# Kernel optimization log

Measured on AMD Instinct MI355X. Metric: run time of the kernel, lower is better.

The kernel has to match this reference:

```python
import jax, jax.numpy as jnp
import numpy as np

B, H, W, C = 8, 64, 64, 256
C8 = C // 8  # query/key channels


def setup_inputs() -> dict:
    key = jax.random.key(0)
    ks = jax.random.split(key, 8)
    s = 0.02  # init scale for weights
    return {
        "x": jax.random.normal(ks[0], (B, H, W, C), dtype=jnp.float32),
        "Wq": jax.random.normal(ks[1], (C, C8), dtype=jnp.float32) * s,
        "bq": jnp.zeros((C8,), dtype=jnp.float32),
        "Wk": jax.random.normal(ks[2], (C, C8), dtype=jnp.float32) * s,
        "bk": jnp.zeros((C8,), dtype=jnp.float32),
        "Wv": jax.random.normal(ks[3], (C, C), dtype=jnp.float32) * s,
        "bv": jnp.zeros((C,), dtype=jnp.float32),
        "gamma": jnp.full((1,), 0.5, dtype=jnp.float32),
    }


def reference(x, Wq, bq, Wk, bk, Wv, bv, gamma):
    Bn, Hn, Wn, Cn = x.shape
    N = Hn * Wn
    xf = x.reshape(Bn, N, Cn)            # flatten spatial dims: [B, N, C]
    # 1x1 convs == per-pixel dense projections over channels
    q = xf @ Wq + bq                     # [B, N, C//8]
    k = xf @ Wk + bk                     # [B, N, C//8]
    v = xf @ Wv + bv                     # [B, N, C]
    # energy[b,i,j] = k_i . q_j  (matches tf.matmul(key, query, transpose_b=True))
    energy = jnp.einsum('bic,bjc->bij', k, q)   # [B, N, N]
    attn = jax.nn.softmax(energy, axis=-1)      # softmax over last axis
    # out_i = sum_j attn[i,j] * v_j  (intended SAGAN aggregation in NHWC layout)
    out = jnp.einsum('bij,bjc->bic', attn, v)   # [B, N, C]
    out = out.reshape(Bn, Hn, Wn, Cn)
    return gamma * out + x
```

## Files before the change

### kernel.cpp

```cpp
#include <hip/hip_runtime.h>

typedef __attribute__((ext_vector_type(8))) short short8;
typedef __attribute__((ext_vector_type(4))) float f32x4;
typedef __attribute__((ext_vector_type(16))) float f32x16;
typedef __attribute__((ext_vector_type(2))) unsigned int u32x2;
typedef __attribute__((ext_vector_type(4))) unsigned int u32x4;
typedef unsigned short u16;
typedef unsigned int u32;

#define MFMA16(a, b, c) __builtin_amdgcn_mfma_f32_16x16x32_bf16((a), (b), (c), 0, 0, 0)
#define MFMA32(a, b, c) __builtin_amdgcn_mfma_f32_32x32x16_bf16((a), (b), (c), 0, 0, 0)

#define BAR_VMEM() asm volatile("s_waitcnt vmcnt(0) lgkmcnt(0)\ns_barrier" ::: "memory")
#define BAR_LDS()  asm volatile("s_waitcnt lgkmcnt(0)\ns_barrier" ::: "memory")

#define BATCH 8
#define NTOK 4096
#define CDIM 256
#define CQK 32
#define LOG2E 1.4426950408889634f

__device__ __forceinline__ u16 f2bf(float f) {
  u32 u = __float_as_uint(f);
  return (u16)((u + 0x7FFFu + ((u >> 16) & 1u)) >> 16);
}
__device__ __forceinline__ u32 pack2(float a, float b) {
  const u32 ua = __float_as_uint(a) + 0x8000u;
  const u32 ub = __float_as_uint(b) + 0x8000u;
#if __has_builtin(__builtin_amdgcn_perm)
  return __builtin_amdgcn_perm(ub, ua, 0x07060302u);
#else
  return (ua >> 16) | (ub & 0xFFFF0000u);
#endif
}
__device__ __forceinline__ float fexp2(float x) {
#if __has_builtin(__builtin_amdgcn_exp2f)
  return __builtin_amdgcn_exp2f(x);
#else
  return exp2f(x);
#endif
}
__device__ __forceinline__ void gl_lds16(const u16* g, u16* l) {
  __builtin_amdgcn_global_load_lds(
      (const __attribute__((address_space(1))) unsigned int*)(g),
      (__attribute__((address_space(3))) unsigned int*)(l), 16, 0, 0);
}

__global__ void k_prep(const float* __restrict__ Wq, const float* __restrict__ bq,
                       const float* __restrict__ Wk, const float* __restrict__ bk,
                       const float* __restrict__ Wv, const float* __restrict__ bv,
                       u16* __restrict__ wtf, float* __restrict__ bias) {
  const int f = blockIdx.x;
  const int L = threadIdx.x;
  const int ct = f >> 3, ks = f & 7;
  const int o = ct * 16 + (L & 15);
  const int ch = ks * 32 + (L >> 4) * 8;
  short8 v8;
#pragma unroll
  for (int jj = 0; jj < 8; jj++) {
    const int c = ch + jj;
    float v;
    if (o < 32)       v = Wq[c * CQK + o];
    else if (o < 64)  v = Wk[c * CQK + (o - 32)];
    else              v = Wv[c * CDIM + (o - 64)];
    v8[jj] = (short)f2bf(v);
  }
  *(short8*)(wtf + (size_t)f * 512 + L * 8) = v8;
  if (f == 0) {
    for (int i = L; i < 320; i += 64) {
      if (i < 32)      bias[i] = bq[i];
      else if (i < 64) bias[i] = bk[i - 32];
      else             bias[i] = bv[i - 64];
    }
  }
}

__global__ __launch_bounds__(256, 2) void k_proj(
    const float* __restrict__ x, const u16* __restrict__ wtf,
    const float* __restrict__ bias,
    u16* __restrict__ q_ws, u16* __restrict__ k_ws, u16* __restrict__ vt_ws) {
  __shared__ u16 x_lds[64 * 264];
  __shared__ u16 vt_t[64 * 72];
  const int m0 = blockIdx.x * 64;
  const int tid = threadIdx.x;
  const int w = tid >> 6, L = tid & 63;
  const int lr = L & 15, q4 = L >> 4;

  short8 wfA[5], wfB[5];
#pragma unroll
  for (int j = 0; j < 5; j++)
    wfA[j] = *(const short8*)(wtf + ((size_t)((j * 4 + w) * 8 + 0)) * 512 + L * 8);

#pragma unroll
  for (int ii = 0; ii < 8; ii++) {
    const int e = (tid + 256 * ii) * 8;
    const int row = e >> 8, col = e & 255;
    const float* src = x + (size_t)(m0 + row) * CDIM + col;
    f32x4 a = *(const f32x4*)src;
    f32x4 b4 = *(const f32x4*)(src + 4);
    u32x4 pk;
    pk[0] = pack2(a[0], a[1]);
    pk[1] = pack2(a[2], a[3]);
    pk[2] = pack2(b4[0], b4[1]);
    pk[3] = pack2(b4[2], b4[3]);
    *(u32x4*)&x_lds[row * 264 + col] = pk;
  }
  __syncthreads();

  f32x4 acc[4][5];
#pragma unroll
  for (int rg = 0; rg < 4; rg++)
#pragma unroll
    for (int j = 0; j < 5; j++) acc[rg][j] = (f32x4){0.f, 0.f, 0.f, 0.f};

#pragma unroll
  for (int ks = 0; ks < 8; ks++) {
    if (ks < 7) {
#pragma unroll
      for (int j = 0; j < 5; j++) {
        short8 v = *(const short8*)(wtf +
            ((size_t)((j * 4 + w) * 8 + ks + 1)) * 512 + L * 8);
        if (ks & 1) wfA[j] = v; else wfB[j] = v;
      }
    }
#pragma unroll
    for (int rg = 0; rg < 4; rg++) {
      short8 a = *(const short8*)&x_lds[(rg * 16 + lr) * 264 + ks * 32 + q4 * 8];
#pragma unroll
      for (int j = 0; j < 5; j++)
        acc[rg][j] = MFMA16(a, (ks & 1) ? wfB[j] : wfA[j], acc[rg][j]);
    }
  }

  {
    const float bb = bias[w * 16 + lr];
#pragma unroll
    for (int rg = 0; rg < 4; rg++)
#pragma unroll
      for (int r = 0; r < 4; r++) {
        const int row = m0 + rg * 16 + q4 * 4 + r;
        float v = acc[rg][0][r] + bb;
        if (w < 2) q_ws[(size_t)row * CQK + w * 16 + lr] = f2bf(v);
        else       k_ws[(size_t)row * CQK + (w - 2) * 16 + lr] = f2bf(v * LOG2E);
      }
  }
  const int b = m0 >> 12, nloc = m0 & 4095;
  const int rb2 = ((lr >> 3) & 1) << 2;
  const int c_l = w * 16 + lr;
#pragma unroll
  for (int cg = 0; cg < 4; cg++) {
    __syncthreads();
    const int j = cg + 1;
    const float bb = bias[(4 + cg * 4 + w) * 16 + lr];
#pragma unroll
    for (int rg = 0; rg < 4; rg++) {
      const int n_base = (rg * 16 + q4 * 4) ^ rb2;
      u32x2 pk;
      pk[0] = pack2(acc[rg][j][0] + bb, acc[rg][j][1] + bb);
      pk[1] = pack2(acc[rg][j][2] + bb, acc[rg][j][3] + bb);
      *(u32x2*)&vt_t[c_l * 72 + n_base] = pk;
    }
    __syncthreads();
#pragma unroll
    for (int i = 0; i < 2; i++) {
      const int gch = tid + 256 * i;
      const int cl2 = gch >> 3, jc = gch & 7;
      short8 v = *(const short8*)&vt_t[cl2 * 72 + jc * 8];
      *(short8*)(vt_ws + ((size_t)(b * CDIM + cg * 64 + cl2)) * NTOK + nloc + jc * 8) = v;
    }
  }
}

__global__ __launch_bounds__(256, 2) void k_attn(
    const float* __restrict__ x, const u16* __restrict__ q_ws,
    const u16* __restrict__ k_ws, const u16* __restrict__ vt_ws,
    const float* __restrict__ gamma, float* __restrict__ out) {
  __shared__ u16 vt_lds[2][256 * 64];
  __shared__ u16 p_lds[64 * 64];

  const int bid = blockIdx.x;
  const int b = bid & 7;
  const int it = bid >> 3;
  const int i0 = it * 64;
  const int tid = threadIdx.x;
  const int w = tid >> 6, L = tid & 63;
  const int lr = L & 15, q4 = L >> 4;
  const int L31 = L & 31, Lhi = L >> 5, L7 = L & 7;

  const short8 a_k = *(const short8*)(k_ws +
      ((size_t)(b * NTOK + i0 + w * 16 + lr)) * CQK + q4 * 8);

  const int cl_base = tid >> 3;
  const int jc_sw = (tid & 7) ^ (cl_base & 7);
  const u16* vt_g = vt_ws + ((size_t)(b * CDIM + cl_base)) * NTOK + jc_sw * 8;
  const u16* q_base = q_ws + (size_t)b * NTOK * CQK;

  f32x16 o_acc[2][2];
#pragma unroll
  for (int ih = 0; ih < 2; ih++)
#pragma unroll
    for (int ct2 = 0; ct2 < 2; ct2++)
#pragma unroll
      for (int e = 0; e < 16; e++) o_acc[ih][ct2][e] = 0.f;
  float lsum = 0.f;

  u16* pw0 = p_lds + (w * 16 + lr) * 64 + (((q4 & 1) ^ ((lr >> 3) & 1)) << 2);
  const int q4h = q4 >> 1;

  short8 bqA[4], bqB[4];
#pragma unroll
  for (int t = 0; t < 4; t++)
    bqA[t] = *(const short8*)(q_base + (size_t)(t * 16 + lr) * CQK + q4 * 8);
#pragma unroll
  for (int ii = 0; ii < 8; ii++)
    gl_lds16(vt_g + (size_t)(ii * 32) * NTOK, &vt_lds[0][ii * 2048 + w * 512]);

#define ATTN_ITER(JT, VB_CUR, VB_NXT, BQ, BQN)                                   \
  do {                                                                           \
    const int j0 = (JT) * 64;                                                    \
    BAR_LDS();                         \
                             \
    f32x4 s[4];                                                                  \
    _Pragma("unroll")                                                            \
    for (int t = 0; t < 4; t++)                                                  \
      s[t] = MFMA16(BQ[t], a_k, ((f32x4){0.f, 0.f, 0.f, 0.f}));                  \
                   \
    _Pragma("unroll")                                                            \
    for (int t = 0; t < 4; t++) {                                                \
      const float p0 = fexp2(s[t][0]);                                           \
      const float p1 = fexp2(s[t][1]);                                           \
      const float p2 = fexp2(s[t][2]);                                           \
      const float p3 = fexp2(s[t][3]);                                           \
      lsum += (p0 + p1) + (p2 + p3);                                             \
      u32x2 pk;                                                                  \
      pk[0] = pack2(p0, p1);                                                     \
      pk[1] = pack2(p2, p3);                                                     \
      *(u32x2*)(pw0 + (((2 * t + q4h) ^ (lr & 7)) * 8)) = pk;                    \
    }                                                                            \
    BAR_VMEM();          \
             \
    if ((JT) < 63) {                                                             \
      _Pragma("unroll")                                                          \
      for (int ii = 0; ii < 8; ii++)                                             \
        gl_lds16(vt_g + (size_t)(ii * 32) * NTOK + (j0 + 64),                    \
                 &VB_NXT[ii * 2048 + w * 512]);                                  \
    }                                                                            \
    _Pragma("unroll")                                                            \
    for (int t = 0; t < 4; t++)                                                  \
      BQN[t] = *(const short8*)(q_base +                                         \
               (size_t)(j0 + 64 + t * 16 + lr) * CQK + q4 * 8);                  \
             \
    _Pragma("unroll")                                                            \
    for (int ks = 0; ks < 4; ks++) {                                             \
      const int slot = (((ks * 2 + Lhi) ^ L7)) * 8;                              \
      short8 a_p0 = *(const short8*)(p_lds + L31 * 64 + slot);                   \
      short8 a_p1 = *(const short8*)(p_lds + (32 + L31) * 64 + slot);            \
      _Pragma("unroll")                                                          \
      for (int ct2 = 0; ct2 < 2; ct2++) {                                        \
        const int cl = w * 64 + ct2 * 32 + L31;                                  \
        short8 b_v = *(const short8*)(VB_CUR + cl * 64 + slot);                  \
        o_acc[0][ct2] = MFMA32(a_p0, b_v, o_acc[0][ct2]);                        \
        o_acc[1][ct2] = MFMA32(a_p1, b_v, o_acc[1][ct2]);                        \
      }                                                                          \
    }                                                                            \
  } while (0)

  for (int jt2 = 0; jt2 < 64; jt2 += 2) {
    ATTN_ITER(jt2,     vt_lds[0], vt_lds[1], bqA, bqB);
    ATTN_ITER(jt2 + 1, vt_lds[1], vt_lds[0], bqB, bqA);
  }
#undef ATTN_ITER

  float s2 = lsum;
  s2 += __shfl_xor(s2, 16);
  s2 += __shfl_xor(s2, 32);
  const float rl = 1.0f / s2;
  BAR_LDS();
  float* lp = (float*)p_lds;
  if (q4 == 0) lp[w * 16 + lr] = rl;
  BAR_LDS();

  float linv2[2][16];
#pragma unroll
  for (int ih = 0; ih < 2; ih++)
#pragma unroll
    for (int rg = 0; rg < 16; rg++)
      linv2[ih][rg] = lp[ih * 32 + (rg & 3) + 8 * (rg >> 2) + 4 * Lhi];

  const float g = gamma[0];
#pragma unroll
  for (int ih = 0; ih < 2; ih++)
#pragma unroll
    for (int ct2 = 0; ct2 < 2; ct2++) {
      const int c = w * 64 + ct2 * 32 + L31;
#pragma unroll
      for (int rg = 0; rg < 16; rg++) {
        const int i = i0 + ih * 32 + (rg & 3) + 8 * (rg >> 2) + 4 * Lhi;
        const size_t idx = ((size_t)(b * NTOK + i)) * CDIM + c;
        out[idx] = g * (o_acc[ih][ct2][rg] * linv2[ih][rg]) + x[idx];
      }
    }
}

extern "C" void kernel_launch(void* const* d_in, const int* in_sizes, int n_in,
                              void* d_out, int out_size, void* d_ws, size_t ws_size,
                              hipStream_t stream) {
  const float* x  = (const float*)d_in[0];
  const float* Wq = (const float*)d_in[1];
  const float* bq = (const float*)d_in[2];
  const float* Wk = (const float*)d_in[3];
  const float* bk = (const float*)d_in[4];
  const float* Wv = (const float*)d_in[5];
  const float* bv = (const float*)d_in[6];
  const float* gamma = (const float*)d_in[7];
  float* out = (float*)d_out;

  char* ws = (char*)d_ws;
  u16* q_ws  = (u16*)(ws);
  u16* k_ws  = (u16*)(ws + (2u << 20));
  u16* vt_ws = (u16*)(ws + (4u << 20));
  u16* wtf   = (u16*)(ws + (20u << 20));
  float* bias = (float*)(ws + (20u << 20) + (256u << 10));

  k_prep<<<160, 64, 0, stream>>>(Wq, bq, Wk, bk, Wv, bv, wtf, bias);
  k_proj<<<512, 256, 0, stream>>>(x, wtf, bias, q_ws, k_ws, vt_ws);
  k_attn<<<512, 256, 0, stream>>>(x, q_ws, k_ws, vt_ws, gamma, out);
}
```

Baseline: 196.8 us.

## Software-pipeline QK^T/exp of next tile with PV MFMAs via double-buffered P

Double-buffers the P tile in LDS so the score MFMAs and exp/pack for tile j+1 are interleaved with the PV MFMA loop of tile j. This drops one barrier per iteration and lets VALU exp work overlap matrix-core work. Adds a prologue and epilogue and an extra 8KB of LDS, which could affect occupancy at 2 blocks per CU.

```diff
diff --git a/kernel.cpp b/kernel.cpp
--- a/kernel.cpp
+++ b/kernel.cpp
@@ -176,7 +176,7 @@
     const u16* __restrict__ k_ws, const u16* __restrict__ vt_ws,
     const float* __restrict__ gamma, float* __restrict__ out) {
   __shared__ u16 vt_lds[2][256 * 64];
-  __shared__ u16 p_lds[64 * 64];
+  __shared__ u16 p_lds[2][64 * 64];
 
   const int bid = blockIdx.x;
   const int b = bid & 7;
@@ -204,8 +204,23 @@
       for (int e = 0; e < 16; e++) o_acc[ih][ct2][e] = 0.f;
   float lsum = 0.f;
 
-  u16* pw0 = p_lds + (w * 16 + lr) * 64 + (((q4 & 1) ^ ((lr >> 3) & 1)) << 2);
+  const int pw_off = (w * 16 + lr) * 64 + (((q4 & 1) ^ ((lr >> 3) & 1)) << 2);
   const int q4h = q4 >> 1;
+  u16* const pl0 = &p_lds[0][0];
+  u16* const pl1 = &p_lds[1][0];
+
+#define EXPW(SV, T, PW)                                                          \
+  do {                                                                           \
+    const float p0 = fexp2((SV)[0]);                                             \
+    const float p1 = fexp2((SV)[1]);                                             \
+    const float p2 = fexp2((SV)[2]);                                             \
+    const float p3 = fexp2((SV)[3]);                                             \
+    lsum += (p0 + p1) + (p2 + p3);                                               \
+    u32x2 pk;                                                                    \
+    pk[0] = pack2(p0, p1);                                                       \
+    pk[1] = pack2(p2, p3);                                                       \
+    *(u32x2*)((PW) + (((2 * (T) + q4h) ^ (lr & 7)) * 8)) = pk;                   \
+  } while (0)
 
   short8 bqA[4], bqB[4];
 #pragma unroll
@@ -214,69 +229,90 @@
 #pragma unroll
   for (int ii = 0; ii < 8; ii++)
     gl_lds16(vt_g + (size_t)(ii * 32) * NTOK, &vt_lds[0][ii * 2048 + w * 512]);
-
-#define ATTN_ITER(JT, VB_CUR, VB_NXT, BQ, BQN)                                   \
+  {
+    f32x4 s0 = MFMA16(bqA[0], a_k, ((f32x4){0.f, 0.f, 0.f, 0.f}));
+    f32x4 s1 = MFMA16(bqA[1], a_k, ((f32x4){0.f, 0.f, 0.f, 0.f}));
+    f32x4 s2 = MFMA16(bqA[2], a_k, ((f32x4){0.f, 0.f, 0.f, 0.f}));
+    f32x4 s3 = MFMA16(bqA[3], a_k, ((f32x4){0.f, 0.f, 0.f, 0.f}));
+    u16* pwn = pl0 + pw_off;
+    EXPW(s0, 0, pwn);
+    EXPW(s1, 1, pwn);
+    EXPW(s2, 2, pwn);
+    EXPW(s3, 3, pwn);
+  }
+#pragma unroll
+  for (int t = 0; t < 4; t++)
+    bqB[t] = *(const short8*)(q_base + (size_t)(64 + t * 16 + lr) * CQK + q4 * 8);
+
+#define ATTN_ITER(JT, PL_CUR, PL_NXT, VB_CUR, VB_NXT, BQN, BQF, DO_Q)            \
   do {                                                                           \
     const int j0 = (JT) * 64;                                                    \
-    BAR_LDS();                         \
-                             \
-    f32x4 s[4];                                                                  \
+    BAR_VMEM();    \
     _Pragma("unroll")                                                            \
-    for (int t = 0; t < 4; t++)                                                  \
-      s[t] = MFMA16(BQ[t], a_k, ((f32x4){0.f, 0.f, 0.f, 0.f}));                  \
-                   \
-    _Pragma("unroll")                                                            \
-    for (int t = 0; t < 4; t++) {                                                \
-      const float p0 = fexp2(s[t][0]);                                           \
-      const float p1 = fexp2(s[t][1]);                                           \
-      const float p2 = fexp2(s[t][2]);                                           \
-      const float p3 = fexp2(s[t][3]);                                           \
-      lsum += (p0 + p1) + (p2 + p3);                                             \
-      u32x2 pk;                                                                  \
-      pk[0] = pack2(p0, p1);                                                     \
-      pk[1] = pack2(p2, p3);                                                     \
-      *(u32x2*)(pw0 + (((2 * t + q4h) ^ (lr & 7)) * 8)) = pk;                    \
-    }                                                                            \
-    BAR_VMEM();          \
-             \
-    if ((JT) < 63) {                                                             \
-      _Pragma("unroll")                                                          \
-      for (int ii = 0; ii < 8; ii++)                                             \
-        gl_lds16(vt_g + (size_t)(ii * 32) * NTOK + (j0 + 64),                    \
-                 &VB_NXT[ii * 2048 + w * 512]);                                  \
-    }                                                                            \
-    _Pragma("unroll")                                                            \
-    for (int t = 0; t < 4; t++)                                                  \
-      BQN[t] = *(const short8*)(q_base +                                         \
-               (size_t)(j0 + 64 + t * 16 + lr) * CQK + q4 * 8);                  \
-             \
+    for (int ii = 0; ii < 8; ii++)                                               \
+      gl_lds16(vt_g + (size_t)(ii * 32) * NTOK + (j0 + 64),                      \
+               &VB_NXT[ii * 2048 + w * 512]);                                    \
+       \
+    f32x4 s0 = MFMA16(BQN[0], a_k, ((f32x4){0.f, 0.f, 0.f, 0.f}));               \
+    f32x4 s1 = MFMA16(BQN[1], a_k, ((f32x4){0.f, 0.f, 0.f, 0.f}));               \
+    f32x4 s2 = MFMA16(BQN[2], a_k, ((f32x4){0.f, 0.f, 0.f, 0.f}));               \
+    f32x4 s3 = MFMA16(BQN[3], a_k, ((f32x4){0.f, 0.f, 0.f, 0.f}));               \
+    u16* pwn = (PL_NXT) + pw_off;                                                \
+            \
     _Pragma("unroll")                                                            \
     for (int ks = 0; ks < 4; ks++) {                                             \
       const int slot = (((ks * 2 + Lhi) ^ L7)) * 8;                              \
-      short8 a_p0 = *(const short8*)(p_lds + L31 * 64 + slot);                   \
-      short8 a_p1 = *(const short8*)(p_lds + (32 + L31) * 64 + slot);            \
+      short8 a_p0 = *(const short8*)((PL_CUR) + L31 * 64 + slot);                \
+      short8 a_p1 = *(const short8*)((PL_CUR) + (32 + L31) * 64 + slot);         \
       _Pragma("unroll")                                                          \
       for (int ct2 = 0; ct2 < 2; ct2++) {                                        \
         const int cl = w * 64 + ct2 * 32 + L31;                                  \
-        short8 b_v = *(const short8*)(VB_CUR + cl * 64 + slot);                  \
+        short8 b_v = *(const short8*)((VB_CUR) + cl * 64 + slot);                \
         o_acc[0][ct2] = MFMA32(a_p0, b_v, o_acc[0][ct2]);                        \
         o_acc[1][ct2] = MFMA32(a_p1, b_v, o_acc[1][ct2]);                        \
       }                                                                          \
+      if (ks == 0) EXPW(s0, 0, pwn);                                             \
+      if (ks == 1) EXPW(s1, 1, pwn);                                             \
+      if (ks == 2) EXPW(s2, 2, pwn);                                             \
+      if (ks == 3) EXPW(s3, 3, pwn);                                             \
+    }                                                                            \
+    if (DO_Q) {                                                                  \
+      _Pragma("unroll")                                                          \
+      for (int t = 0; t < 4; t++)                                                \
+        BQF[t] = *(const short8*)(q_base +                                       \
+                 (size_t)(j0 + 128 + t * 16 + lr) * CQK + q4 * 8);               \
     }                                                                            \
   } while (0)
 
-  for (int jt2 = 0; jt2 < 64; jt2 += 2) {
-    ATTN_ITER(jt2,     vt_lds[0], vt_lds[1], bqA, bqB);
-    ATTN_ITER(jt2 + 1, vt_lds[1], vt_lds[0], bqB, bqA);
-  }
+  for (int jt2 = 0; jt2 < 62; jt2 += 2) {
+    ATTN_ITER(jt2,     pl0, pl1, (&vt_lds[0][0]), (&vt_lds[1][0]), bqB, bqA, 1);
+    ATTN_ITER(jt2 + 1, pl1, pl0, (&vt_lds[1][0]), (&vt_lds[0][0]), bqA, bqB, 1);
+  }
+  ATTN_ITER(62, pl0, pl1, (&vt_lds[0][0]), (&vt_lds[1][0]), bqB, bqA, 0);
 #undef ATTN_ITER
+
+  BAR_VMEM();
+#pragma unroll
+  for (int ks = 0; ks < 4; ks++) {
+    const int slot = (((ks * 2 + Lhi) ^ L7)) * 8;
+    short8 a_p0 = *(const short8*)(pl1 + L31 * 64 + slot);
+    short8 a_p1 = *(const short8*)(pl1 + (32 + L31) * 64 + slot);
+#pragma unroll
+    for (int ct2 = 0; ct2 < 2; ct2++) {
+      const int cl = w * 64 + ct2 * 32 + L31;
+      short8 b_v = *(const short8*)(&vt_lds[1][0] + cl * 64 + slot);
+      o_acc[0][ct2] = MFMA32(a_p0, b_v, o_acc[0][ct2]);
+      o_acc[1][ct2] = MFMA32(a_p1, b_v, o_acc[1][ct2]);
+    }
+  }
+#undef EXPW
 
   float s2 = lsum;
   s2 += __shfl_xor(s2, 16);
   s2 += __shfl_xor(s2, 32);
   const float rl = 1.0f / s2;
   BAR_LDS();
-  float* lp = (float*)p_lds;
+  float* lp = (float*)pl0;
   if (q4 == 0) lp[w * 16 + lr] = rl;
   BAR_LDS();
 
```

Result: no change. 195.3 us (-0.8%).

## Drop LDS staging in attention; prepack V into MFMA fragment layout

Applied to the files above, without the earlier changes.

The projection kernel now writes V in a pre-swizzled per-fragment layout, so the attention kernel can load MFMA B operands straight from global memory into registers. The attention loop computes scores with 32x32 MFMAs, exponentiates them and feeds P directly as the A operand from registers. This removes the P and V round trips through LDS and all per-iteration barriers. Each wave computes its own scores redundantly instead of sharing them, and the change depends on global load latency being hidden by register prefetching.

```diff
diff --git a/kernel.cpp b/kernel.cpp
--- a/kernel.cpp
+++ b/kernel.cpp
@@ -10,9 +10,6 @@
 
 #define MFMA16(a, b, c) __builtin_amdgcn_mfma_f32_16x16x32_bf16((a), (b), (c), 0, 0, 0)
 #define MFMA32(a, b, c) __builtin_amdgcn_mfma_f32_32x32x16_bf16((a), (b), (c), 0, 0, 0)
-
-#define BAR_VMEM() asm volatile("s_waitcnt vmcnt(0) lgkmcnt(0)\ns_barrier" ::: "memory")
-#define BAR_LDS()  asm volatile("s_waitcnt lgkmcnt(0)\ns_barrier" ::: "memory")
 
 #define BATCH 8
 #define NTOK 4096
@@ -39,11 +36,6 @@
 #else
   return exp2f(x);
 #endif
-}
-__device__ __forceinline__ void gl_lds16(const u16* g, u16* l) {
-  __builtin_amdgcn_global_load_lds(
-      (const __attribute__((address_space(1))) unsigned int*)(g),
-      (__attribute__((address_space(3))) unsigned int*)(l), 16, 0, 0);
 }
 
 __global__ void k_prep(const float* __restrict__ Wq, const float* __restrict__ bq,
@@ -80,7 +72,7 @@
     const float* __restrict__ bias,
     u16* __restrict__ q_ws, u16* __restrict__ k_ws, u16* __restrict__ vt_ws) {
   __shared__ u16 x_lds[64 * 264];
-  __shared__ u16 vt_t[64 * 72];
+  __shared__ u16 vt_t[64 * 76];
   const int m0 = blockIdx.x * 64;
   const int tid = threadIdx.x;
   const int w = tid >> 6, L = tid & 63;
@@ -144,8 +136,7 @@
         else       k_ws[(size_t)row * CQK + (w - 2) * 16 + lr] = f2bf(v * LOG2E);
       }
   }
-  const int b = m0 >> 12, nloc = m0 & 4095;
-  const int rb2 = ((lr >> 3) & 1) << 2;
+  const int b = m0 >> 12, nt = (m0 & 4095) >> 6;
   const int c_l = w * 16 + lr;
 #pragma unroll
   for (int cg = 0; cg < 4; cg++) {
@@ -154,19 +145,26 @@
     const float bb = bias[(4 + cg * 4 + w) * 16 + lr];
 #pragma unroll
     for (int rg = 0; rg < 4; rg++) {
-      const int n_base = (rg * 16 + q4 * 4) ^ rb2;
       u32x2 pk;
       pk[0] = pack2(acc[rg][j][0] + bb, acc[rg][j][1] + bb);
       pk[1] = pack2(acc[rg][j][2] + bb, acc[rg][j][3] + bb);
-      *(u32x2*)&vt_t[c_l * 72 + n_base] = pk;
+      *(u32x2*)&vt_t[c_l * 76 + rg * 16 + q4 * 4] = pk;
     }
     __syncthreads();
 #pragma unroll
     for (int i = 0; i < 2; i++) {
       const int gch = tid + 256 * i;
-      const int cl2 = gch >> 3, jc = gch & 7;
-      short8 v = *(const short8*)&vt_t[cl2 * 72 + jc * 8];
-      *(short8*)(vt_ws + ((size_t)(b * CDIM + cg * 64 + cl2)) * NTOK + nloc + jc * 8) = v;
+      const int fid = gch >> 6;
+      const int lane = gch & 63;
+      const int jt = fid >> 2, kh = (fid >> 1) & 1, ct2 = fid & 1;
+      const int cc = ct2 * 32 + (lane & 31);
+      const int n0 = jt * 32 + kh * 16 + (lane >> 5) * 4;
+      u32x2 va = *(const u32x2*)&vt_t[cc * 76 + n0];
+      u32x2 vb2 = *(const u32x2*)&vt_t[cc * 76 + n0 + 8];
+      u32x4 vv = {va[0], va[1], vb2[0], vb2[1]};
+      *(short8*)(vt_ws +
+          ((((size_t)(b * 64 + nt) * 4 + cg) * 8 + fid) * 512) + lane * 8) =
+          __builtin_bit_cast(short8, vv);
     }
   }
 }
@@ -175,131 +173,128 @@
     const float* __restrict__ x, const u16* __restrict__ q_ws,
     const u16* __restrict__ k_ws, const u16* __restrict__ vt_ws,
     const float* __restrict__ gamma, float* __restrict__ out) {
-  __shared__ u16 vt_lds[2][256 * 64];
-  __shared__ u16 p_lds[64 * 64];
+  __shared__ float lp4[4][64];
 
   const int bid = blockIdx.x;
   const int b = bid & 7;
-  const int it = bid >> 3;
-  const int i0 = it * 64;
+  const int i0 = (bid >> 3) * 64;
   const int tid = threadIdx.x;
   const int w = tid >> 6, L = tid & 63;
-  const int lr = L & 15, q4 = L >> 4;
-  const int L31 = L & 31, Lhi = L >> 5, L7 = L & 7;
-
-  const short8 a_k = *(const short8*)(k_ws +
-      ((size_t)(b * NTOK + i0 + w * 16 + lr)) * CQK + q4 * 8);
-
-  const int cl_base = tid >> 3;
-  const int jc_sw = (tid & 7) ^ (cl_base & 7);
-  const u16* vt_g = vt_ws + ((size_t)(b * CDIM + cl_base)) * NTOK + jc_sw * 8;
-  const u16* q_base = q_ws + (size_t)b * NTOK * CQK;
-
-  f32x16 o_acc[2][2];
+  const int L31 = L & 31, Lhi = L >> 5;
+
+  const u16* kb = k_ws + ((size_t)(b * NTOK + i0 + L31)) * CQK + Lhi * 8;
+  const u16* qb = q_ws + ((size_t)(b * NTOK) + L31) * CQK + Lhi * 8;
+  const u16* vb = vt_ws + ((size_t)b << 20) + w * 4096 + (size_t)L * 8;
+
+  f32x16 z16;
+#pragma unroll
+  for (int e = 0; e < 16; e++) z16[e] = 0.f;
+  f32x16 o00 = z16, o01 = z16, o10 = z16, o11 = z16;
+  float ls0 = 0.f, ls1 = 0.f;
+
+  short8 vV0 = *(const short8*)(vb + 0 * 512);
+  short8 vV1 = *(const short8*)(vb + 1 * 512);
+  short8 vV2 = *(const short8*)(vb + 2 * 512);
+  short8 vV3 = *(const short8*)(vb + 3 * 512);
+  short8 vV4 = *(const short8*)(vb + 4 * 512);
+  short8 vV5 = *(const short8*)(vb + 5 * 512);
+  short8 vV6 = *(const short8*)(vb + 6 * 512);
+  short8 vV7 = *(const short8*)(vb + 7 * 512);
+  const short8 kf00 = *(const short8*)(kb);
+  const short8 kf01 = *(const short8*)(kb + 16);
+  const short8 kf10 = *(const short8*)(kb + 32 * CQK);
+  const short8 kf11 = *(const short8*)(kb + 32 * CQK + 16);
+  short8 q00 = *(const short8*)(qb);
+  short8 q01 = *(const short8*)(qb + 16);
+  short8 q10 = *(const short8*)(qb + 32 * CQK);
+  short8 q11 = *(const short8*)(qb + 32 * CQK + 16);
+
+#define EPPV(SV, V0, V1, V2, V3, OA, OB, LS)                                   \
+  do {                                                                         \
+    float e0 = fexp2((SV)[0]), e1 = fexp2((SV)[1]);                            \
+    float e2 = fexp2((SV)[2]), e3 = fexp2((SV)[3]);                            \
+    float e4 = fexp2((SV)[4]), e5 = fexp2((SV)[5]);                            \
+    float e6 = fexp2((SV)[6]), e7 = fexp2((SV)[7]);                            \
+    float e8 = fexp2((SV)[8]), e9 = fexp2((SV)[9]);                            \
+    float e10 = fexp2((SV)[10]), e11 = fexp2((SV)[11]);                        \
+    float e12 = fexp2((SV)[12]), e13 = fexp2((SV)[13]);                        \
+    float e14 = fexp2((SV)[14]), e15 = fexp2((SV)[15]);                        \
+    LS += ((((e0 + e1) + (e2 + e3)) + ((e4 + e5) + (e6 + e7))) +               \
+           (((e8 + e9) + (e10 + e11)) + ((e12 + e13) + (e14 + e15))));         \
+    u32x4 pA = {pack2(e0, e1), pack2(e2, e3), pack2(e4, e5), pack2(e6, e7)};   \
+    u32x4 pB = {pack2(e8, e9), pack2(e10, e11), pack2(e12, e13),               \
+                pack2(e14, e15)};                                              \
+    const short8 a0 = __builtin_bit_cast(short8, pA);                          \
+    const short8 a1 = __builtin_bit_cast(short8, pB);                          \
+    OA = MFMA32(a0, V0, OA);                                                   \
+    OB = MFMA32(a0, V1, OB);                                                   \
+    OA = MFMA32(a1, V2, OA);                                                   \
+    OB = MFMA32(a1, V3, OB);                                                   \
+  } while (0)
+
+#define UNIT(QA, QB, KA, KB, V0, V1, V2, V3, OA, OB, LS)                       \
+  do {                                                                         \
+    f32x16 sv_ = MFMA32(QA, KA, z16);                                          \
+    sv_ = MFMA32(QB, KB, sv_);                                                 \
+    EPPV(sv_, V0, V1, V2, V3, OA, OB, LS);                                     \
+  } while (0)
+
+  for (int t = 0; t < 64; ++t) {
+    const size_t vn = (size_t)(t + 1) * 16384;
+    UNIT(q00, q01, kf00, kf01, vV0, vV1, vV2, vV3, o00, o01, ls0);
+    UNIT(q10, q11, kf00, kf01, vV4, vV5, vV6, vV7, o00, o01, ls0);
+    UNIT(q00, q01, kf10, kf11, vV0, vV1, vV2, vV3, o10, o11, ls1);
+    vV0 = *(const short8*)(vb + vn + 0 * 512);
+    vV1 = *(const short8*)(vb + vn + 1 * 512);
+    vV2 = *(const short8*)(vb + vn + 2 * 512);
+    vV3 = *(const short8*)(vb + vn + 3 * 512);
+    f32x16 svz = MFMA32(q10, kf10, z16);
+    svz = MFMA32(q11, kf11, svz);
+    {
+      const size_t qo = (size_t)(t + 1) * 64 * CQK;
+      q00 = *(const short8*)(qb + qo);
+      q01 = *(const short8*)(qb + qo + 16);
+      q10 = *(const short8*)(qb + qo + 32 * CQK);
+      q11 = *(const short8*)(qb + qo + 32 * CQK + 16);
+    }
+    EPPV(svz, vV4, vV5, vV6, vV7, o10, o11, ls1);
+    vV4 = *(const short8*)(vb + vn + 4 * 512);
+    vV5 = *(const short8*)(vb + vn + 5 * 512);
+    vV6 = *(const short8*)(vb + vn + 6 * 512);
+    vV7 = *(const short8*)(vb + vn + 7 * 512);
+  }
+#undef UNIT
+#undef EPPV
+
+  ls0 += __shfl_xor(ls0, 32);
+  ls1 += __shfl_xor(ls1, 32);
+  if (L < 32) {
+    lp4[w][L] = 1.0f / ls0;
+    lp4[w][32 + L] = 1.0f / ls1;
+  }
+  asm volatile("s_waitcnt lgkmcnt(0)" ::: "memory");
+
+  float linv[2][16];
 #pragma unroll
   for (int ih = 0; ih < 2; ih++)
 #pragma unroll
-    for (int ct2 = 0; ct2 < 2; ct2++)
-#pragma unroll
-      for (int e = 0; e < 16; e++) o_acc[ih][ct2][e] = 0.f;
-  float lsum = 0.f;
-
-  u16* pw0 = p_lds + (w * 16 + lr) * 64 + (((q4 & 1) ^ ((lr >> 3) & 1)) << 2);
-  const int q4h = q4 >> 1;
-
-  short8 bqA[4], bqB[4];
-#pragma unroll
-  for (int t = 0; t < 4; t++)
-    bqA[t] = *(const short8*)(q_base + (size_t)(t * 16 + lr) * CQK + q4 * 8);
-#pragma unroll
-  for (int ii = 0; ii < 8; ii++)
-    gl_lds16(vt_g + (size_t)(ii * 32) * NTOK, &vt_lds[0][ii * 2048 + w * 512]);
-
-#define ATTN_ITER(JT, VB_CUR, VB_NXT, BQ, BQN)                                   \
-  do {                                                                           \
-    const int j0 = (JT) * 64;                                                    \
-    BAR_LDS();                         \
-                             \
-    f32x4 s[4];                                                                  \
-    _Pragma("unroll")                                                            \
-    for (int t = 0; t < 4; t++)                                                  \
-      s[t] = MFMA16(BQ[t], a_k, ((f32x4){0.f, 0.f, 0.f, 0.f}));                  \
-                   \
-    _Pragma("unroll")                                                            \
-    for (int t = 0; t < 4; t++) {                                                \
-      const float p0 = fexp2(s[t][0]);                                           \
-      const float p1 = fexp2(s[t][1]);                                           \
-      const float p2 = fexp2(s[t][2]);                                           \
-      const float p3 = fexp2(s[t][3]);                                           \
-      lsum += (p0 + p1) + (p2 + p3);                                             \
-      u32x2 pk;                                                                  \
-      pk[0] = pack2(p0, p1);                                                     \
-      pk[1] = pack2(p2, p3);                                                     \
-      *(u32x2*)(pw0 + (((2 * t + q4h) ^ (lr & 7)) * 8)) = pk;                    \
-    }                                                                            \
-    BAR_VMEM();          \
-             \
-    if ((JT) < 63) {                                                             \
-      _Pragma("unroll")                                                          \
-      for (int ii = 0; ii < 8; ii++)                                             \
-        gl_lds16(vt_g + (size_t)(ii * 32) * NTOK + (j0 + 64),                    \
-                 &VB_NXT[ii * 2048 + w * 512]);                                  \
-    }                                                                            \
-    _Pragma("unroll")                                                            \
-    for (int t = 0; t < 4; t++)                                                  \
-      BQN[t] = *(const short8*)(q_base +                                         \
-               (size_t)(j0 + 64 + t * 16 + lr) * CQK + q4 * 8);                  \
-             \
-    _Pragma("unroll")                                                            \
-    for (int ks = 0; ks < 4; ks++) {                                             \
-      const int slot = (((ks * 2 + Lhi) ^ L7)) * 8;                              \
-      short8 a_p0 = *(const short8*)(p_lds + L31 * 64 + slot);                   \
-      short8 a_p1 = *(const short8*)(p_lds + (32 + L31) * 64 + slot);            \
-      _Pragma("unroll")                                                          \
-      for (int ct2 = 0; ct2 < 2; ct2++) {                                        \
-        const int cl = w * 64 + ct2 * 32 + L31;                                  \
-        short8 b_v = *(const short8*)(VB_CUR + cl * 64 + slot);                  \
-        o_acc[0][ct2] = MFMA32(a_p0, b_v, o_acc[0][ct2]);                        \
-        o_acc[1][ct2] = MFMA32(a_p1, b_v, o_acc[1][ct2]);                        \
-      }                                                                          \
-    }                                                                            \
-  } while (0)
-
-  for (int jt2 = 0; jt2 < 64; jt2 += 2) {
-    ATTN_ITER(jt2,     vt_lds[0], vt_lds[1], bqA, bqB);
-    ATTN_ITER(jt2 + 1, vt_lds[1], vt_lds[0], bqB, bqA);
-  }
-#undef ATTN_ITER
-
-  float s2 = lsum;
-  s2 += __shfl_xor(s2, 16);
-  s2 += __shfl_xor(s2, 32);
-  const float rl = 1.0f / s2;
-  BAR_LDS();
-  float* lp = (float*)p_lds;
-  if (q4 == 0) lp[w * 16 + lr] = rl;
-  BAR_LDS();
-
-  float linv2[2][16];
-#pragma unroll
-  for (int ih = 0; ih < 2; ih++)
-#pragma unroll
     for (int rg = 0; rg < 16; rg++)
-      linv2[ih][rg] = lp[ih * 32 + (rg & 3) + 8 * (rg >> 2) + 4 * Lhi];
+      linv[ih][rg] = lp4[w][ih * 32 + (rg & 3) + 8 * (rg >> 2) + 4 * Lhi];
 
   const float g = gamma[0];
-#pragma unroll
-  for (int ih = 0; ih < 2; ih++)
-#pragma unroll
-    for (int ct2 = 0; ct2 < 2; ct2++) {
-      const int c = w * 64 + ct2 * 32 + L31;
-#pragma unroll
-      for (int rg = 0; rg < 16; rg++) {
-        const int i = i0 + ih * 32 + (rg & 3) + 8 * (rg >> 2) + 4 * Lhi;
-        const size_t idx = ((size_t)(b * NTOK + i)) * CDIM + c;
-        out[idx] = g * (o_acc[ih][ct2][rg] * linv2[ih][rg]) + x[idx];
-      }
-    }
+#define STO(OV, IH, CT2)                                                       \
+  _Pragma("unroll")                                                            \
+  for (int rg = 0; rg < 16; rg++) {                                            \
+    const int i = i0 + (IH) * 32 + (rg & 3) + 8 * (rg >> 2) + 4 * Lhi;         \
+    const int c = w * 64 + (CT2) * 32 + L31;                                   \
+    const size_t idx = ((size_t)(b * NTOK + i)) * CDIM + c;                    \
+    out[idx] = g * (OV[rg] * linv[IH][rg]) + x[idx];                           \
+  }
+  STO(o00, 0, 0)
+  STO(o01, 0, 1)
+  STO(o10, 1, 0)
+  STO(o11, 1, 1)
+#undef STO
 }
 
 extern "C" void kernel_launch(void* const* d_in, const int* in_sizes, int n_in,
```

Measured after the change: 214.3 us. 1.09x slower.
